# Kernel tuning notes

Hardware: AMD Instinct MI355X
Metric: run time of the kernel (lower is better)

The kernel has to match this reference:

```python
import jax, jax.numpy as jnp
import numpy as np

B, N, C, H = 2, 2048, 1024, 16
D = C // H  # head_dim = 64


def setup_inputs() -> dict:
    key = jax.random.key(0)
    ks = jax.random.split(key, 5)
    s = 0.02
    return {
        "x": jax.random.normal(ks[0], (B, N, C), dtype=jnp.float32),
        "w_qkv": jax.random.normal(ks[1], (3 * C, C), dtype=jnp.float32) * s,
        "b_qkv": jnp.zeros((3 * C,), dtype=jnp.float32),
        "w_proj": jax.random.normal(ks[2], (C, C), dtype=jnp.float32) * s,
        "b_proj": jnp.zeros((C,), dtype=jnp.float32),
    }


def reference(x, w_qkv, b_qkv, w_proj, b_proj):
    scale = D ** -0.5
    # QKV projection: [B,N,3C]
    qkv = jnp.einsum('bnc,oc->bno', x, w_qkv) + b_qkv
    qkv = qkv.reshape(B, N, 3, H, D).transpose(2, 0, 3, 1, 4)  # [3,B,H,N,D]
    q, k, v = qkv[0], qkv[1], qkv[2]
    attn = jnp.einsum('bhnd,bhmd->bhnm', q, k) * scale  # [B,H,N,N]
    attn = jax.nn.softmax(attn, axis=-1)
    out = jnp.einsum('bhnm,bhmd->bhnd', attn, v)  # [B,H,N,D]
    out = out.transpose(0, 2, 1, 3).reshape(B, N, C)
    return jnp.einsum('bnc,oc->bno', out, w_proj) + b_proj
```

## Files before the change

kernel.cpp:

```cpp
#include <hip/hip_runtime.h>
#include <hip/hip_bf16.h>

typedef __attribute__((ext_vector_type(4))) float f32x4;
typedef __attribute__((ext_vector_type(16))) float f32x16;
typedef __attribute__((ext_vector_type(8))) short short8;
typedef __attribute__((ext_vector_type(4))) unsigned int u32x4;
typedef __attribute__((ext_vector_type(2))) unsigned int u32x2;
typedef unsigned short u16;

__device__ __forceinline__ u16 f2bf(float x) {
  unsigned u = __float_as_uint(x);
  u += 0x7fffu + ((u >> 16) & 1u);
  return (u16)(u >> 16);
}

__device__ __forceinline__ void gload_lds16(const void* g, void* l) {
  __builtin_amdgcn_global_load_lds(
      (__attribute__((address_space(1))) void*)g,
      (__attribute__((address_space(3))) void*)l, 16, 0, 0);
}

__global__ void cvt_all(const float* __restrict__ x, const float* __restrict__ wq,
                        const float* __restrict__ wp, ushort4* __restrict__ dst) {
  const int N1 = 1048576, N2 = 786432, NT = 2097152;
  for (int i = blockIdx.x * 256 + threadIdx.x; i < NT; i += 524288) {
    float4 v;
    if (i < N1)            v = ((const float4*)x)[i];
    else if (i < N1 + N2)  v = ((const float4*)wq)[i - N1];
    else                   v = ((const float4*)wp)[i - N1 - N2];
    ushort4 o;
    o.x = f2bf(v.x); o.y = f2bf(v.y); o.z = f2bf(v.z); o.w = f2bf(v.w);
    dst[i] = o;
  }
}

__global__ __launch_bounds__(512, 2) void gemm256_bt(
    const u16* __restrict__ A, const u16* __restrict__ B,
    const float* __restrict__ bias, u16* __restrict__ Cout,
    int M, int N, int K, int nbx)
{
  __shared__ u16 LA[2][2][8192];
  __shared__ u16 LB[2][2][8192];

  const int tid  = threadIdx.x;
  const int w    = tid >> 6;
  const int lane = tid & 63;
  const int wm   = w >> 2;
  const int wn   = w & 3;
  const int hi   = lane >> 4;
  const int lo   = lane & 15;

  const int L  = (int)(blockIdx.x & 7) * ((int)gridDim.x >> 3) + (int)(blockIdx.x >> 3);
  const int bx = L / 16, by = L % 16;
  const long brow = (long)by * 256;
  const long bcol = (long)bx * 256;

  f32x4 acc[8][4];
#pragma unroll
  for (int m = 0; m < 8; ++m)
#pragma unroll
    for (int n = 0; n < 4; ++n)
#pragma unroll
      for (int r = 0; r < 4; ++r) acc[m][n][r] = 0.0f;

  const int srow = lane >> 3;
  const int sg   = (lane & 7) ^ srow;
  const int l7   = lo & 7;

  auto stageA = [&](int kt, int bi) {
    const long k0 = (long)kt * 64;
#pragma unroll
    for (int mh = 0; mh < 2; ++mh)
#pragma unroll
      for (int i = 0; i < 2; ++i) {
        const long r = brow + mh * 128 + i * 64 + w * 8 + srow;
        gload_lds16(A + r * K + k0 + sg * 8, &LA[bi][mh][i * 4096 + w * 512]);
      }
  };
  auto stageB = [&](int kt, int bi) {
    const long k0 = (long)kt * 64;
#pragma unroll
    for (int nh = 0; nh < 2; ++nh)
#pragma unroll
      for (int i = 0; i < 2; ++i) {
        const long r = bcol + nh * 128 + i * 64 + w * 8 + srow;
        gload_lds16(B + r * K + k0 + sg * 8, &LB[bi][nh][i * 4096 + w * 512]);
      }
  };

  short8 a[4][2], b0[2][2], b1[2][2];
  auto rdA = [&](int cur, int mq) {
#pragma unroll
    for (int f = 0; f < 4; ++f) {
      const int rl = mq * 64 + f * 16 + lo;
#pragma unroll
      for (int ks = 0; ks < 2; ++ks)
        a[f][ks] = *(const short8*)(&LA[cur][wm][rl * 64 + ((ks * 4 + hi) ^ l7) * 8]);
    }
  };
  auto rdB = [&](int cur, int nq, short8 bb[2][2]) {
#pragma unroll
    for (int f = 0; f < 2; ++f) {
      const int rl = (wn & 1) * 64 + nq * 32 + f * 16 + lo;
#pragma unroll
      for (int ks = 0; ks < 2; ++ks)
        bb[f][ks] = *(const short8*)(&LB[cur][wn >> 1][rl * 64 + ((ks * 4 + hi) ^ l7) * 8]);
    }
  };

#define MFMA16(mq, nq, BB)                                                          \
  __builtin_amdgcn_s_setprio(1);                                                    \
  _Pragma("unroll")                                                                 \
  for (int f = 0; f < 4; ++f)                                                       \
    _Pragma("unroll")                                                               \
    for (int n = 0; n < 2; ++n)                                                     \
      _Pragma("unroll")                                                             \
      for (int ks = 0; ks < 2; ++ks)                                                \
        acc[(mq)*4 + f][(nq)*2 + n] = __builtin_amdgcn_mfma_f32_16x16x32_bf16(      \
            a[f][ks], BB[n][ks], acc[(mq)*4 + f][(nq)*2 + n], 0, 0, 0);             \
  __builtin_amdgcn_s_setprio(0);

#define PHASE_WAIT()                                      \
  __builtin_amdgcn_s_barrier();                           \
  asm volatile("s_waitcnt lgkmcnt(0)" ::: "memory");      \
  __builtin_amdgcn_sched_barrier(0);

  const int nkt = K >> 6;
  stageA(0, 0); stageB(0, 0);
  asm volatile("s_waitcnt vmcnt(0)" ::: "memory");
  __builtin_amdgcn_s_barrier();
  int cur = 0;

  for (int kt = 0; kt < nkt; ++kt) {
    const bool pf = (kt + 1 < nkt);
    rdA(cur, 0); rdB(cur, 0, b0);
    if (pf) stageA(kt + 1, cur ^ 1);
    PHASE_WAIT();
    MFMA16(0, 0, b0);
    __builtin_amdgcn_s_barrier();
    rdB(cur, 1, b1);
    if (pf) stageB(kt + 1, cur ^ 1);
    PHASE_WAIT();
    MFMA16(0, 1, b1);
    __builtin_amdgcn_s_barrier();
    rdA(cur, 1);
    PHASE_WAIT();
    MFMA16(1, 0, b0);
    __builtin_amdgcn_s_barrier();
    MFMA16(1, 1, b1);
    if (pf) { asm volatile("s_waitcnt vmcnt(0)" ::: "memory"); }
    __builtin_amdgcn_sched_barrier(0);
    __builtin_amdgcn_s_barrier();
    cur ^= 1;
  }
#undef MFMA16
#undef PHASE_WAIT

  const float qsc = (bcol < 1024) ? 0.18033688011112042f : 1.0f;
  float bv[4];
#pragma unroll
  for (int n = 0; n < 4; ++n) bv[n] = bias[bcol + wn * 64 + n * 16 + lo];
#pragma unroll
  for (int m = 0; m < 8; ++m)
#pragma unroll
    for (int n = 0; n < 4; ++n)
#pragma unroll
      for (int r = 0; r < 4; ++r) {
        const long row = brow + wm * 128 + m * 16 + hi * 4 + r;
        const long col = bcol + wn * 64 + n * 16 + lo;
        Cout[row * (long)N + col] = f2bf((acc[m][n][r] + bv[n]) * qsc);
      }
}

template<int OUT_BF16>
__global__ __launch_bounds__(256) void gemm_bt(
    const u16* __restrict__ A, const u16* __restrict__ B,
    const float* __restrict__ bias, void* __restrict__ Cout,
    int M, int N, int K)
{
  __shared__ u16 As[2][128 * 64];
  __shared__ u16 Bs[2][128 * 64];
  const int tid  = threadIdx.x;
  const int lane = tid & 63;
  const int w    = tid >> 6;
  const int wm   = w >> 1, wn = w & 1;
  const int hi   = lane >> 4;
  const int lo   = lane & 15;
  const int l7   = lo & 7;
  const long brow = (long)blockIdx.y * 128;
  const long bcol = (long)blockIdx.x * 128;

  f32x4 acc[4][4];
#pragma unroll
  for (int i = 0; i < 4; i++)
#pragma unroll
    for (int j = 0; j < 4; j++)
#pragma unroll
      for (int r = 0; r < 4; r++) acc[i][j][r] = 0.0f;

  const int srow = lane >> 3;
  const int sg   = (lane & 7) ^ srow;

  float bv[4];
#pragma unroll
  for (int fn = 0; fn < 4; fn++) bv[fn] = bias[bcol + wn * 64 + fn * 16 + lo];

  auto stage = [&](int kt, int bi) {
    const int k0 = kt << 6;
#pragma unroll
    for (int c = 0; c < 4; ++c) {
      const int chunk = (c << 2) + w;
      const int ra = (chunk << 3) + srow;
      gload_lds16(A + (size_t)(brow + ra) * K + k0 + sg * 8, &As[bi][chunk * 512]);
      gload_lds16(B + (size_t)(bcol + ra) * K + k0 + sg * 8, &Bs[bi][chunk * 512]);
    }
  };

  const int nkt = K >> 6;
  stage(0, 0);
  __syncthreads();
  int cur = 0;

  for (int kt = 0; kt < nkt; ++kt) {
    if (kt + 1 < nkt) stage(kt + 1, cur ^ 1);
#pragma unroll
    for (int ks = 0; ks < 2; ++ks) {
      short8 af[4], bfr[4];
      const int g = ((ks * 4 + hi) ^ l7) * 8;
#pragma unroll
      for (int f = 0; f < 4; f++) {
        af[f]  = *(const short8*)(&As[cur][(wm * 64 + f * 16 + lo) * 64 + g]);
        bfr[f] = *(const short8*)(&Bs[cur][(wn * 64 + f * 16 + lo) * 64 + g]);
      }
#pragma unroll
      for (int fm = 0; fm < 4; fm++)
#pragma unroll
        for (int fn = 0; fn < 4; fn++)
          acc[fm][fn] = __builtin_amdgcn_mfma_f32_16x16x32_bf16(af[fm], bfr[fn], acc[fm][fn], 0, 0, 0);
    }
    __syncthreads();
    cur ^= 1;
  }

#pragma unroll
  for (int fm = 0; fm < 4; fm++)
#pragma unroll
    for (int fn = 0; fn < 4; fn++)
#pragma unroll
      for (int r = 0; r < 4; r++) {
        const long row = brow + wm * 64 + fm * 16 + hi * 4 + r;
        const long col = bcol + wn * 64 + fn * 16 + lo;
        const float v = acc[fm][fn][r] + bv[fn];
        if (OUT_BF16) ((u16*)Cout)[row * (long)N + col] = f2bf(v);
        else          ((float*)Cout)[row * (long)N + col] = v;
      }
}

__global__ __launch_bounds__(512, 4) void attn_fused(
    const u16* __restrict__ qkv, u16* __restrict__ out)
{
  __shared__ __align__(16) char smem[65536];

  const int tid  = threadIdx.x;
  const int w    = tid >> 6;
  const int lane = tid & 63;
  const int l31  = lane & 31;
  const int hc   = lane >> 5;
  const int g1   = (lane >> 4) & 1;
  const int l15  = lane & 15;
  const int half = w >> 2;
  const int qg   = w & 3;

  const int bid  = blockIdx.x;
  const int xcd  = bid & 7;
  const int slot = bid >> 3;
  const int qb   = slot & 15;
  const int bh   = ((slot >> 4) << 3) | xcd;
  const int b    = bh >> 4, h = bh & 15;

  short8 qf[4];
  {
    const u16* qp = qkv + (size_t)(b * 2048 + qb * 128 + qg * 32 + l31) * 3072 + h * 64 + hc * 8;
#pragma unroll
    for (int ds = 0; ds < 4; ++ds) qf[ds] = *(const short8*)(qp + ds * 16);
  }

  f32x16 acc0, acc1;
#pragma unroll
  for (int r = 0; r < 16; ++r) { acc0[r] = 0.f; acc1[r] = 0.f; }
  float lsum = 0.f;

  const int srow8 = lane >> 3;
  const int kgl   = (lane & 7) ^ srow8;
  const int vkey  = (lane >> 5) * 4 + ((lane >> 1) & 3);
  const int vd    = ((lane >> 3) & 3) * 16 + (lane & 1) * 8;

  auto kbuf = [&](int bi) { return (u16*)(smem + (size_t)(half * 2 + bi) * 8192); };
  auto vbuf = [&](int bi) { return (u16*)(smem + 32768 + (size_t)(half * 2 + bi) * 8192); };

  auto stage = [&](int t, int bi) {
    const size_t rbase = (size_t)(b * 2048 + half * 1024 + t * 64);
    u16* Kb = kbuf(bi);
    u16* Vb = vbuf(bi);
#pragma unroll
    for (int c = 0; c < 2; ++c) {
      const int chunk = qg * 2 + c;
      gload_lds16(qkv + (rbase + chunk * 8 + srow8) * 3072 + 1024 + h * 64 + kgl * 8,
                  Kb + chunk * 512);
      gload_lds16(qkv + (rbase + chunk * 8 + vkey) * 3072 + 2048 + h * 64 + vd,
                  Vb + chunk * 512);
    }
  };

  stage(0, 0);
  __syncthreads();
  int cur = 0;

  for (int t = 0; t < 16; ++t) {
    if (t < 15) stage(t + 1, cur ^ 1);

    const u16* Kc = kbuf(cur);
    const unsigned va =
        (unsigned)(unsigned long long)(const __attribute__((address_space(3))) u16*)vbuf(cur);

    f32x16 s0, s1;
#pragma unroll
    for (int r = 0; r < 16; ++r) { s0[r] = 0.f; s1[r] = 0.f; }
    __builtin_amdgcn_s_setprio(1);
#pragma unroll
    for (int ds = 0; ds < 4; ++ds) {
      const int gb = (((2 * ds + hc) ^ (lane & 7)) << 4);
      const short8 k0 = *(const short8*)((const char*)Kc + l31 * 128 + gb);
      const short8 k1 = *(const short8*)((const char*)Kc + 4096 + l31 * 128 + gb);
      s0 = __builtin_amdgcn_mfma_f32_32x32x16_bf16(k0, qf[ds], s0, 0, 0, 0);
      s1 = __builtin_amdgcn_mfma_f32_32x32x16_bf16(k1, qf[ds], s1, 0, 0, 0);
    }
    __builtin_amdgcn_s_setprio(0);

    float p[32];
#pragma unroll
    for (int r = 0; r < 16; ++r) {
      p[r]      = __builtin_amdgcn_exp2f(s0[r]);
      p[16 + r] = __builtin_amdgcn_exp2f(s1[r]);
    }
    {
      float a0 = 0.f, a1 = 0.f, a2 = 0.f, a3 = 0.f;
#pragma unroll
      for (int r = 0; r < 8; ++r) {
        a0 += p[r]; a1 += p[8 + r]; a2 += p[16 + r]; a3 += p[24 + r];
      }
      lsum += (a0 + a1) + (a2 + a3);
    }

    short8 pa[4];
#pragma unroll
    for (int ks = 0; ks < 4; ++ks) {
      const int bs = ks * 8;
      unsigned X0, X1, X2, X3;
      asm("v_cvt_pk_bf16_f32 %0, %1, %2" : "=v"(X0) : "v"(p[bs + 0]), "v"(p[bs + 1]));
      asm("v_cvt_pk_bf16_f32 %0, %1, %2" : "=v"(X1) : "v"(p[bs + 2]), "v"(p[bs + 3]));
      asm("v_cvt_pk_bf16_f32 %0, %1, %2" : "=v"(X2) : "v"(p[bs + 4]), "v"(p[bs + 5]));
      asm("v_cvt_pk_bf16_f32 %0, %1, %2" : "=v"(X3) : "v"(p[bs + 6]), "v"(p[bs + 7]));
      asm("v_permlane32_swap_b32 %0, %1" : "+v"(X0), "+v"(X2));
      asm("v_permlane32_swap_b32 %0, %1" : "+v"(X1), "+v"(X3));
      u32x4 wv;
      wv[0] = X0; wv[1] = X1; wv[2] = X2; wv[3] = X3;
      pa[ks] = __builtin_bit_cast(short8, wv);
    }

#pragma unroll
    for (int dt = 0; dt < 2; ++dt) {
      const unsigned vb = va + (unsigned)(hc * 1024 + dt * 256 + g1 * 128 + l15 * 8);
      u32x2 q0, q1, q2, q3, q4, q5, q6, q7;
      asm volatile("ds_read_b64_tr_b16 %0, %1"             : "=v"(q0) : "v"(vb));
      asm volatile("ds_read_b64_tr_b16 %0, %1 offset:512"  : "=v"(q1) : "v"(vb));
      asm volatile("ds_read_b64_tr_b16 %0, %1 offset:2048" : "=v"(q2) : "v"(vb));
      asm volatile("ds_read_b64_tr_b16 %0, %1 offset:2560" : "=v"(q3) : "v"(vb));
      asm volatile("ds_read_b64_tr_b16 %0, %1 offset:4096" : "=v"(q4) : "v"(vb));
      asm volatile("ds_read_b64_tr_b16 %0, %1 offset:4608" : "=v"(q5) : "v"(vb));
      asm volatile("ds_read_b64_tr_b16 %0, %1 offset:6144" : "=v"(q6) : "v"(vb));
      asm volatile("ds_read_b64_tr_b16 %0, %1 offset:6656" : "=v"(q7) : "v"(vb));
      asm volatile("s_waitcnt lgkmcnt(0)" ::: "memory");
      __builtin_amdgcn_sched_barrier(0);
      __builtin_amdgcn_s_setprio(1);
      f32x16 A = dt ? acc1 : acc0;
      {
        u32x4 bb; bb[0] = q0[0]; bb[1] = q0[1]; bb[2] = q1[0]; bb[3] = q1[1];
        A = __builtin_amdgcn_mfma_f32_32x32x16_bf16(pa[0], __builtin_bit_cast(short8, bb), A, 0, 0, 0);
      }
      {
        u32x4 bb; bb[0] = q2[0]; bb[1] = q2[1]; bb[2] = q3[0]; bb[3] = q3[1];
        A = __builtin_amdgcn_mfma_f32_32x32x16_bf16(pa[1], __builtin_bit_cast(short8, bb), A, 0, 0, 0);
      }
      {
        u32x4 bb; bb[0] = q4[0]; bb[1] = q4[1]; bb[2] = q5[0]; bb[3] = q5[1];
        A = __builtin_amdgcn_mfma_f32_32x32x16_bf16(pa[2], __builtin_bit_cast(short8, bb), A, 0, 0, 0);
      }
      {
        u32x4 bb; bb[0] = q6[0]; bb[1] = q6[1]; bb[2] = q7[0]; bb[3] = q7[1];
        A = __builtin_amdgcn_mfma_f32_32x32x16_bf16(pa[3], __builtin_bit_cast(short8, bb), A, 0, 0, 0);
      }
      __builtin_amdgcn_s_setprio(0);
      if (dt) acc1 = A; else acc0 = A;
    }

    __syncthreads();
    cur ^= 1;
  }

  float ltot = lsum + __shfl_xor(lsum, 32);
  float* MG = (float*)smem;
  const int midx = (qg * 64 + lane) * 33;
  if (half == 1) {
#pragma unroll
    for (int r = 0; r < 16; ++r) { MG[midx + r] = acc0[r]; MG[midx + 16 + r] = acc1[r]; }
    MG[midx + 32] = ltot;
  }
  __syncthreads();
  if (half == 0) {
#pragma unroll
    for (int r = 0; r < 16; ++r) { acc0[r] += MG[midx + r]; acc1[r] += MG[midx + 16 + r]; }
    ltot += MG[midx + 32];
    const float inv = 1.0f / ltot;
    const size_t orow0 = (size_t)(b * 2048 + qb * 128 + qg * 32);
#pragma unroll
    for (int r = 0; r < 16; ++r) {
      const int rowq = (r & 3) + 8 * (r >> 2) + 4 * hc;
      const float ir = __shfl(inv, rowq);
      out[(orow0 + rowq) * 1024 + h * 64 + l31]      = f2bf(acc0[r] * ir);
      out[(orow0 + rowq) * 1024 + h * 64 + 32 + l31] = f2bf(acc1[r] * ir);
    }
  }
}

extern "C" void kernel_launch(void* const* d_in, const int* in_sizes, int n_in,
                              void* d_out, int out_size, void* d_ws, size_t ws_size,
                              hipStream_t stream) {
  const float* x      = (const float*)d_in[0];
  const float* w_qkv  = (const float*)d_in[1];
  const float* b_qkv  = (const float*)d_in[2];
  const float* w_proj = (const float*)d_in[3];
  const float* b_proj = (const float*)d_in[4];
  float* out = (float*)d_out;

  char* ws = (char*)d_ws;
  u16* xb     = (u16*)(ws);
  u16* wqkvb  = (u16*)(ws + (8ull  << 20));
  u16* wprojb = (u16*)(ws + (14ull << 20));
  u16* qkvb   = (u16*)(ws + (16ull << 20));
  u16* aob    = (u16*)(ws + (40ull << 20));

  cvt_all<<<2048, 256, 0, stream>>>(x, w_qkv, w_proj, (ushort4*)ws);

  gemm256_bt<<<192, 512, 0, stream>>>(xb, wqkvb, b_qkv, qkvb, 4096, 3072, 1024, 12);

  attn_fused<<<512, 512, 0, stream>>>(qkvb, aob);

  gemm_bt<0><<<dim3(8, 32), 256, 0, stream>>>(aob, wprojb, b_proj, out, 4096, 1024, 1024);
}
```

Before: 113.0 us.

## Prefetch two k-tiles ahead in QKV GEMM with partial vmcnt waits

Restructures the QKV projection GEMM main loop to keep two k-tiles in flight. The loop is unrolled by two over fixed LDS buffers, and global-to-LDS loads for tile t+2 are spread across the compute phases after each region has been read. The full vmcnt(0) drain is replaced by vmcnt(8) waits. The goal is to hide global load latency behind MFMA work, with the risk of ordering hazards if the wait counts or barriers are wrong and the assumption that nkt is even.

```diff
diff --git a/kernel.cpp b/kernel.cpp
--- a/kernel.cpp
+++ b/kernel.cpp
@@ -67,44 +67,40 @@
   const int sg   = (lane & 7) ^ srow;
   const int l7   = lo & 7;
 
-  auto stageA = [&](int kt, int bi) {
+  auto stA = [&](int kt, int bi, int i) {
     const long k0 = (long)kt * 64;
 #pragma unroll
-    for (int mh = 0; mh < 2; ++mh)
-#pragma unroll
-      for (int i = 0; i < 2; ++i) {
-        const long r = brow + mh * 128 + i * 64 + w * 8 + srow;
-        gload_lds16(A + r * K + k0 + sg * 8, &LA[bi][mh][i * 4096 + w * 512]);
-      }
-  };
-  auto stageB = [&](int kt, int bi) {
+    for (int mh = 0; mh < 2; ++mh) {
+      const long r = brow + mh * 128 + i * 64 + w * 8 + srow;
+      gload_lds16(A + r * K + k0 + sg * 8, &LA[bi][mh][i * 4096 + w * 512]);
+    }
+  };
+  auto stB = [&](int kt, int bi, int i) {
     const long k0 = (long)kt * 64;
 #pragma unroll
-    for (int nh = 0; nh < 2; ++nh)
-#pragma unroll
-      for (int i = 0; i < 2; ++i) {
-        const long r = bcol + nh * 128 + i * 64 + w * 8 + srow;
-        gload_lds16(B + r * K + k0 + sg * 8, &LB[bi][nh][i * 4096 + w * 512]);
-      }
+    for (int nh = 0; nh < 2; ++nh) {
+      const long r = bcol + nh * 128 + i * 64 + w * 8 + srow;
+      gload_lds16(B + r * K + k0 + sg * 8, &LB[bi][nh][i * 4096 + w * 512]);
+    }
   };
 
   short8 a[4][2], b0[2][2], b1[2][2];
-  auto rdA = [&](int cur, int mq) {
+  auto rdA = [&](int bi, int mq) {
 #pragma unroll
     for (int f = 0; f < 4; ++f) {
       const int rl = mq * 64 + f * 16 + lo;
 #pragma unroll
       for (int ks = 0; ks < 2; ++ks)
-        a[f][ks] = *(const short8*)(&LA[cur][wm][rl * 64 + ((ks * 4 + hi) ^ l7) * 8]);
-    }
-  };
-  auto rdB = [&](int cur, int nq, short8 bb[2][2]) {
+        a[f][ks] = *(const short8*)(&LA[bi][wm][rl * 64 + ((ks * 4 + hi) ^ l7) * 8]);
+    }
+  };
+  auto rdB = [&](int bi, int nq, short8 bb[2][2]) {
 #pragma unroll
     for (int f = 0; f < 2; ++f) {
       const int rl = (wn & 1) * 64 + nq * 32 + f * 16 + lo;
 #pragma unroll
       for (int ks = 0; ks < 2; ++ks)
-        bb[f][ks] = *(const short8*)(&LB[cur][wn >> 1][rl * 64 + ((ks * 4 + hi) ^ l7) * 8]);
+        bb[f][ks] = *(const short8*)(&LB[bi][wn >> 1][rl * 64 + ((ks * 4 + hi) ^ l7) * 8]);
     }
   };
 
@@ -126,32 +122,41 @@
   __builtin_amdgcn_sched_barrier(0);
 
   const int nkt = K >> 6;
-  stageA(0, 0); stageB(0, 0);
-  asm volatile("s_waitcnt vmcnt(0)" ::: "memory");
+  stA(0, 0, 0); stA(0, 0, 1); stB(0, 0, 0); stB(0, 0, 1);
+  stA(1, 1, 0); stA(1, 1, 1); stB(1, 1, 0); stB(1, 1, 1);
+  asm volatile("s_waitcnt vmcnt(8)" ::: "memory");
   __builtin_amdgcn_s_barrier();
-  int cur = 0;
-
-  for (int kt = 0; kt < nkt; ++kt) {
-    const bool pf = (kt + 1 < nkt);
-    rdA(cur, 0); rdB(cur, 0, b0);
-    if (pf) stageA(kt + 1, cur ^ 1);
-    PHASE_WAIT();
-    MFMA16(0, 0, b0);
-    __builtin_amdgcn_s_barrier();
-    rdB(cur, 1, b1);
-    if (pf) stageB(kt + 1, cur ^ 1);
-    PHASE_WAIT();
-    MFMA16(0, 1, b1);
-    __builtin_amdgcn_s_barrier();
-    rdA(cur, 1);
-    PHASE_WAIT();
-    MFMA16(1, 0, b0);
-    __builtin_amdgcn_s_barrier();
+
+  for (int it = 0; it < (nkt >> 1); ++it) {
+    const int t0 = it * 2;
+    const bool pf = (t0 + 2 < nkt);
+    rdA(0, 0); rdB(0, 0, b0);
+    PHASE_WAIT(); MFMA16(0, 0, b0); __builtin_amdgcn_s_barrier();
+    rdB(0, 1, b1);
+    if (pf) stA(t0 + 2, 0, 0);
+    PHASE_WAIT(); MFMA16(0, 1, b1); __builtin_amdgcn_s_barrier();
+    rdA(0, 1);
+    if (pf) stB(t0 + 2, 0, 0);
+    PHASE_WAIT(); MFMA16(1, 0, b0); __builtin_amdgcn_s_barrier();
+    if (pf) { stA(t0 + 2, 0, 1); stB(t0 + 2, 0, 1); }
     MFMA16(1, 1, b1);
-    if (pf) { asm volatile("s_waitcnt vmcnt(0)" ::: "memory"); }
+    if (pf) { asm volatile("s_waitcnt vmcnt(8)" ::: "memory"); }
+    else    { asm volatile("s_waitcnt vmcnt(0)" ::: "memory"); }
     __builtin_amdgcn_sched_barrier(0);
     __builtin_amdgcn_s_barrier();
-    cur ^= 1;
+    rdA(1, 0); rdB(1, 0, b0);
+    PHASE_WAIT(); MFMA16(0, 0, b0); __builtin_amdgcn_s_barrier();
+    rdB(1, 1, b1);
+    if (pf) stA(t0 + 3, 1, 0);
+    PHASE_WAIT(); MFMA16(0, 1, b1); __builtin_amdgcn_s_barrier();
+    rdA(1, 1);
+    if (pf) stB(t0 + 3, 1, 0);
+    PHASE_WAIT(); MFMA16(1, 0, b0); __builtin_amdgcn_s_barrier();
+    if (pf) { stA(t0 + 3, 1, 1); stB(t0 + 3, 1, 1); }
+    MFMA16(1, 1, b1);
+    if (pf) { asm volatile("s_waitcnt vmcnt(8)" ::: "memory"); }
+    __builtin_amdgcn_sched_barrier(0);
+    __builtin_amdgcn_s_barrier();
   }
 #undef MFMA16
 #undef PHASE_WAIT
```

Result: no change. 111.6 us (-1.3%).
